# Kernel optimization log

Hardware: AMD Instinct MI355X
Metric: run time of the kernel (lower is better)

Reference implementation:

```python
import jax, jax.numpy as jnp
import numpy as np

B, T, H = 32, 2048, 1024
NEG = -1e9


def setup_inputs() -> dict:
    key = jax.random.key(0)
    ks = jax.random.split(key, 10)
    s = 1.0 / np.sqrt(H)
    return {
        "query": jax.random.normal(ks[0], (B, T, H), dtype=jnp.float32),
        "key_": jax.random.normal(ks[1], (B, T, H), dtype=jnp.float32),
        "value": jax.random.normal(ks[2], (B, T, H), dtype=jnp.float32),
        "lengths": jax.random.randint(ks[3], (B,), 1, T + 1),
        "Wq": jax.random.uniform(ks[4], (H, H), jnp.float32, -s, s),
        "bq": jax.random.uniform(ks[5], (H,), jnp.float32, -s, s),
        "Wk": jax.random.uniform(ks[6], (H, H), jnp.float32, -s, s),
        "bk": jax.random.uniform(ks[7], (H,), jnp.float32, -s, s),
        "Wz": jax.random.uniform(ks[8], (1, H), jnp.float32, -s, s),
        "bz": jax.random.uniform(ks[9], (1,), jnp.float32, -s, s),
    }


def reference(query, key_, value, lengths, Wq, bq, Wk, bk, Wz, bz):
    # projections: [B,T,H] @ [H,H]^T
    q = jnp.einsum("bth,oh->bto", query, Wq) + bq
    k = jnp.einsum("bth,oh->bto", key_, Wk) + bk
    # additive score -> [B,T,1]
    score = jnp.einsum("bth,oh->bto", jnp.tanh(q + k), Wz) + bz
    # mask positions t >= lengths[b]
    t_idx = jnp.arange(T)[None, :, None]  # [1,T,1]
    mask = t_idx >= lengths[:, None, None]  # [B,T,1]
    score = jnp.where(mask, NEG, score)
    att_weights = jax.nn.softmax(score, axis=1)  # [B,T,1]
    # weights^T [B,1,T] @ value [B,T,H] -> [B,1,H]
    att_value = jnp.einsum("bti,bth->bih", att_weights, value)
    return att_value, att_weights
```

## Files before the change

### kernel.cpp

```cpp
#include <hip/hip_runtime.h>
#include <hip/hip_bf16.h>

constexpr int TSEQ  = 2048;
constexpr int HDIM  = 1024;
constexpr int BATCH = 32;
constexpr int NPART = 16;
constexpr long ROWS = (long)BATCH * TSEQ;

constexpr int GBM = 256, GBN = 256, GBK = 64;
constexpr int GNT = (2 * HDIM) / GBK;

constexpr int BM = 128, BN = 128, BK = 64;
constexpr int NT = (2 * HDIM) / BK;

typedef __attribute__((ext_vector_type(8))) short bf16x8;
typedef __attribute__((ext_vector_type(8))) unsigned short u16x8;
typedef __attribute__((ext_vector_type(4))) float f32x4;

__device__ __forceinline__ unsigned short f2bf(float f) {
    union { float f; unsigned int u; } v; v.f = f;
    unsigned int r = v.u + 0x7FFFu + ((v.u >> 16) & 1u);
    return (unsigned short)(r >> 16);
}

__device__ __forceinline__ void gload16(const unsigned short* g, unsigned short* l) {
    __builtin_amdgcn_global_load_lds(
        (__attribute__((address_space(1))) void*)(g),
        (__attribute__((address_space(3))) void*)(l), 16, 0, 0);
}

__device__ __forceinline__ float fast_tanh(float x) {
    float e = __expf(2.0f * x);
    return 1.0f - 2.0f * __builtin_amdgcn_rcpf(e + 1.0f);
}

__global__ void convert_kernel(const float* __restrict__ q, const float* __restrict__ k,
                               const float* __restrict__ wq, const float* __restrict__ wk,
                               const int* __restrict__ lengths,
                               unsigned short* __restrict__ qb, unsigned short* __restrict__ kb,
                               unsigned short* __restrict__ wqb, unsigned short* __restrict__ wkb) {
    const long GQ = (ROWS * HDIM) / 8;
    const long GW = ((long)HDIM * HDIM) / 8;
    const long TOTAL = 2 * GQ + 2 * GW;
    const long stride = (long)gridDim.x * blockDim.x;
    for (long i = (long)blockIdx.x * blockDim.x + threadIdx.x; i < TOTAL; i += stride) {
        const float* src; unsigned short* dst; long off;
        if (i < 2 * GQ) {
            off = (i < GQ) ? i : i - GQ;
            const int row = (int)(off >> 7);
            if ((row & (TSEQ - 1)) >= lengths[row >> 11]) continue;
            src = (i < GQ) ? q : k;  dst = (i < GQ) ? qb : kb;
        } else if (i < 2 * GQ + GW) { src = wq; dst = wqb; off = i - 2 * GQ; }
        else                        { src = wk; dst = wkb; off = i - 2 * GQ - GW; }
        float4 v0 = *(const float4*)(src + off * 8);
        float4 v1 = *(const float4*)(src + off * 8 + 4);
        u16x8 o;
        o[0] = f2bf(v0.x); o[1] = f2bf(v0.y); o[2] = f2bf(v0.z); o[3] = f2bf(v0.w);
        o[4] = f2bf(v1.x); o[5] = f2bf(v1.y); o[6] = f2bf(v1.z); o[7] = f2bf(v1.w);
        *(u16x8*)(dst + off * 8) = o;
    }
}

__global__ __launch_bounds__(512, 2)
void score_gemm_256(const unsigned short* __restrict__ qb, const unsigned short* __restrict__ kb,
                    const unsigned short* __restrict__ wqb, const unsigned short* __restrict__ wkb,
                    const float* __restrict__ bq, const float* __restrict__ bk,
                    const float* __restrict__ Wz, const int* __restrict__ lengths,
                    float* __restrict__ scorePartial) {
    __shared__ unsigned short As[2 * 2 * 256 * 32];
    __shared__ unsigned short Bs[2 * 2 * 256 * 32];

    const int tid  = threadIdx.x;
    const int lane = tid & 63;
    const int wid  = tid >> 6;
    const int wr   = wid >> 2;
    const int wc   = wid & 3;

    const int x   = (int)blockIdx.x & 7;
    const int j   = (int)blockIdx.x >> 3;
    const int bat = j >> 2;
    const int nb  = j & 3;
    const int mb  = bat * 8 + ((x + bat) & 7);
    const long rowBase = (long)mb * GBM;
    const int  colBase = nb * GBN;

    if (((mb & 7) * GBM) >= lengths[bat]) return;

    const int frow = lane & 15;
    const int cs16 = (((lane >> 4) ^ ((frow >> 1) & 3)) << 4);
    const int sc8  = ((tid & 3) ^ ((tid >> 3) & 3)) * 8;

    f32x4 acc[8][4];
#pragma unroll
    for (int i = 0; i < 8; ++i)
#pragma unroll
        for (int j2 = 0; j2 < 4; ++j2) acc[i][j2] = (f32x4){0.f, 0.f, 0.f, 0.f};

    auto stage_half = [&](int n) {
        if (n >= 4 * GNT) return;
        const int tn   = n >> 2;
        const int part = n & 3;
        const int kh   = part >> 1;
        const int isB  = part & 1;
        const int kglob = tn * GBK + kh * 32;
        const unsigned short* src = (tn < 16) ? (isB ? wqb : qb) : (isB ? wkb : kb);
        const int ksrc = (tn < 16) ? kglob : (kglob - HDIM);
        const long rbase = isB ? (long)colBase : rowBase;
        unsigned short* lds = (isB ? Bs : As) + (tn & 1) * 16384 + kh * 8192;
#pragma unroll
        for (int jj = 0; jj < 2; ++jj) {
            const int row = jj * 128 + (tid >> 2);
            gload16(src + (rbase + row) * (long)HDIM + ksrc + sc8,
                    lds + jj * 4096 + (tid << 3));
        }
    };

    bf16x8 afr[4], bfr[4];
    auto ldA = [&](int d, int kh, int mh) {
        const char* p = (const char*)As + d * 32768 + kh * 16384;
#pragma unroll
        for (int mi = 0; mi < 4; ++mi) {
            const int row = wr * 128 + (mh * 4 + mi) * 16 + frow;
            afr[mi] = *(const bf16x8*)(p + row * 64 + cs16);
        }
    };
    auto ldB = [&](int d, int kh) {
        const char* p = (const char*)Bs + d * 32768 + kh * 16384;
#pragma unroll
        for (int ni = 0; ni < 4; ++ni) {
            const int row = wc * 64 + ni * 16 + frow;
            bfr[ni] = *(const bf16x8*)(p + row * 64 + cs16);
        }
    };

#pragma unroll
    for (int n = 0; n < 6; ++n) stage_half(n);
    asm volatile("s_waitcnt vmcnt(4)" ::: "memory");
    __builtin_amdgcn_s_barrier();

    for (int t = 0; t < GNT; ++t) {
        const int d = t & 1;
#pragma unroll
        for (int q = 0; q < 4; ++q) {
            const int kh = q >> 1, mh = q & 1;
            if (mh == 0) ldB(d, kh);
            ldA(d, kh, mh);
            stage_half(4 * t + q + 6);
            __builtin_amdgcn_s_barrier();
            asm volatile("s_waitcnt lgkmcnt(0)" ::: "memory");
            __builtin_amdgcn_sched_barrier(0);
            __builtin_amdgcn_s_setprio(1);
#pragma unroll
            for (int mi = 0; mi < 4; ++mi)
#pragma unroll
                for (int ni = 0; ni < 4; ++ni)
                    acc[mh * 4 + mi][ni] = __builtin_amdgcn_mfma_f32_16x16x32_bf16(
                        afr[mi], bfr[ni], acc[mh * 4 + mi][ni], 0, 0, 0);
            __builtin_amdgcn_s_setprio(0);
            if (q == 3) {
                if (t < GNT - 2)       asm volatile("s_waitcnt vmcnt(4)" ::: "memory");
                else if (t == GNT - 2) asm volatile("s_waitcnt vmcnt(0)" ::: "memory");
            }
            __builtin_amdgcn_s_barrier();
        }
    }

    float bias[4], wz[4];
#pragma unroll
    for (int ni = 0; ni < 4; ++ni) {
        const int o = colBase + wc * 64 + ni * 16 + frow;
        bias[ni] = bq[o] + bk[o];
        wz[ni]   = Wz[o];
    }
#pragma unroll
    for (int mi = 0; mi < 8; ++mi) {
#pragma unroll
        for (int jj = 0; jj < 4; ++jj) {
            float p = 0.f;
#pragma unroll
            for (int ni = 0; ni < 4; ++ni)
                p += fast_tanh(acc[mi][ni][jj] + bias[ni]) * wz[ni];
#pragma unroll
            for (int off = 1; off < 16; off <<= 1) p += __shfl_xor(p, off);
            if (frow == 0) {
                long r = rowBase + wr * 128 + mi * 16 + (lane >> 4) * 4 + jj;
                scorePartial[r * NPART + nb * 4 + wc] = p;
            }
        }
    }
}

__global__ __launch_bounds__(256, 2)
void score_gemm_fused(const float* __restrict__ query, const float* __restrict__ key_,
                      const float* __restrict__ Wq, const float* __restrict__ Wk,
                      const float* __restrict__ bq, const float* __restrict__ bk,
                      const float* __restrict__ Wz, const int* __restrict__ lengths,
                      float* __restrict__ scorePartial) {
    __shared__ unsigned short As[2][BM * BK];
    __shared__ unsigned short Bs[2][BN * BK];
    const int tid  = threadIdx.x;
    const int lane = tid & 63;
    const int wid  = tid >> 6;
    const int wr   = wid >> 1, wc = wid & 1;
    const int bid = blockIdx.x;
    const int nb  = bid & 7;
    const int mb  = bid >> 3;
    const long rowBase = (long)mb * BM;
    const int  colBase = nb * BN;
    if ((int)(rowBase & (TSEQ - 1)) >= lengths[(int)(rowBase >> 11)]) return;
    const int srow = tid >> 4;
    const int sc   = tid & 15;
    const int rA  = wr * 64 + (lane & 15);
    const int rB  = wc * 64 + (lane & 15);
    const int swz = (lane & 7) << 4;
    const int kb  = (lane >> 4) << 4;

    f32x4 acc[4][4];
#pragma unroll
    for (int i = 0; i < 4; i++)
#pragma unroll
        for (int j = 0; j < 4; j++) acc[i][j] = (f32x4){0.f, 0.f, 0.f, 0.f};

    float4 regA[8], regB[8];
    auto stage_load = [&](int kt) {
        const int kg = kt * BK;
        const float* baseA; const float* baseB; int koff;
        if (kg < HDIM) { baseA = query; baseB = Wq; koff = kg; }
        else           { baseA = key_;  baseB = Wk; koff = kg - HDIM; }
#pragma unroll
        for (int i = 0; i < 8; i++) {
            int row = i * 16 + srow;
            regA[i] = *(const float4*)(baseA + (rowBase + row) * (long)HDIM + koff + sc * 4);
            regB[i] = *(const float4*)(baseB + (long)(colBase + row) * HDIM + koff + sc * 4);
        }
    };
    auto stage_write = [&](int buf) {
#pragma unroll
        for (int i = 0; i < 8; i++) {
            int row = i * 16 + srow;
            int off = row * 128 + (((sc * 8)) ^ ((row & 7) << 4));
            ushort4 ha, hb;
            ha.x = f2bf(regA[i].x); ha.y = f2bf(regA[i].y);
            ha.z = f2bf(regA[i].z); ha.w = f2bf(regA[i].w);
            hb.x = f2bf(regB[i].x); hb.y = f2bf(regB[i].y);
            hb.z = f2bf(regB[i].z); hb.w = f2bf(regB[i].w);
            *(ushort4*)((char*)&As[buf][0] + off) = ha;
            *(ushort4*)((char*)&Bs[buf][0] + off) = hb;
        }
    };
    auto compute = [&](int buf) {
        const char* pA = (const char*)&As[buf][0];
        const char* pB = (const char*)&Bs[buf][0];
        bf16x8 a[4][2], b[4][2];
#pragma unroll
        for (int h = 0; h < 2; h++) {
#pragma unroll
            for (int mi = 0; mi < 4; mi++)
                a[mi][h] = *(const bf16x8*)(pA + (((rA + mi * 16) * 128 + h * 64 + kb) ^ swz));
#pragma unroll
            for (int ni = 0; ni < 4; ni++)
                b[ni][h] = *(const bf16x8*)(pB + (((rB + ni * 16) * 128 + h * 64 + kb) ^ swz));
        }
#pragma unroll
        for (int h = 0; h < 2; h++)
#pragma unroll
            for (int mi = 0; mi < 4; mi++)
#pragma unroll
                for (int ni = 0; ni < 4; ni++)
                    acc[mi][ni] = __builtin_amdgcn_mfma_f32_16x16x32_bf16(
                        a[mi][h], b[ni][h], acc[mi][ni], 0, 0, 0);
    };

    stage_load(0);
    stage_write(0);
    __syncthreads();
    int buf = 0;
    for (int kt = 1; kt < NT; ++kt) {
        stage_load(kt);
        compute(buf);
        stage_write(buf ^ 1);
        __syncthreads();
        buf ^= 1;
    }
    compute(buf);

    float bias[4], wz[4];
#pragma unroll
    for (int ni = 0; ni < 4; ni++) {
        int o = colBase + wc * 64 + ni * 16 + (lane & 15);
        bias[ni] = bq[o] + bk[o];
        wz[ni]   = Wz[o];
    }
#pragma unroll
    for (int mi = 0; mi < 4; mi++) {
#pragma unroll
        for (int j = 0; j < 4; j++) {
            float p = 0.f;
#pragma unroll
            for (int ni = 0; ni < 4; ni++) {
                float s = acc[mi][ni][j] + bias[ni];
                p += fast_tanh(s) * wz[ni];
            }
#pragma unroll
            for (int off = 1; off < 16; off <<= 1) p += __shfl_xor(p, off);
            if ((lane & 15) == 0) {
                long r = rowBase + wr * 64 + mi * 16 + (lane >> 4) * 4 + j;
                scorePartial[r * NPART + nb * 2 + wc] = p;
            }
        }
    }
}

__global__ void softmax_kernel(const float* __restrict__ sp, const float* __restrict__ bzp,
                               const int* __restrict__ lengths,
                               float* __restrict__ w_out, float* __restrict__ w_ws) {
    const int b = blockIdx.x;
    const int tid = threadIdx.x;
    const int len = lengths[b];
    const float bz = bzp[0];
    float sv[8];
    float m = -3.0e38f;
#pragma unroll
    for (int i = 0; i < 8; i++) {
        int t = i * 256 + tid;
        const float4* p = (const float4*)(sp + ((long)b * TSEQ + t) * NPART);
        float s;
        if (t >= len) {
            s = -1e9f;
        } else {
            float4 a = p[0], c = p[1], d = p[2], e = p[3];
            s = (a.x + a.y + a.z + a.w) + (c.x + c.y + c.z + c.w) +
                (d.x + d.y + d.z + d.w) + (e.x + e.y + e.z + e.w) + bz;
        }
        sv[i] = s;
        m = fmaxf(m, s);
    }
    __shared__ float redm[4];
    __shared__ float reds[4];
    for (int off = 32; off; off >>= 1) m = fmaxf(m, __shfl_xor(m, off));
    if ((tid & 63) == 0) redm[tid >> 6] = m;
    __syncthreads();
    m = fmaxf(fmaxf(redm[0], redm[1]), fmaxf(redm[2], redm[3]));
    float sum = 0.f;
    float ev[8];
#pragma unroll
    for (int i = 0; i < 8; i++) {
        ev[i] = expf(sv[i] - m);
        sum += ev[i];
    }
    for (int off = 32; off; off >>= 1) sum += __shfl_xor(sum, off);
    if ((tid & 63) == 0) reds[tid >> 6] = sum;
    __syncthreads();
    sum = reds[0] + reds[1] + reds[2] + reds[3];
    const float inv = 1.0f / sum;
#pragma unroll
    for (int i = 0; i < 8; i++) {
        int t = i * 256 + tid;
        float w = ev[i] * inv;
        w_out[(long)b * TSEQ + t] = w;
        w_ws[(long)b * TSEQ + t] = w;
    }
}

__global__ void pv_partial(const float* __restrict__ w, const float* __restrict__ value,
                           const int* __restrict__ lengths, float* __restrict__ part) {
    const int ntc = gridDim.x;
    const int tchunk = TSEQ / ntc;
    const int tc = blockIdx.x;
    const int hc = blockIdx.y;
    const int b  = blockIdx.z;
    const int tid = threadIdx.x;
    const int h = hc * 512 + tid * 4;
    float* dst = part + ((long)(b * ntc + tc)) * HDIM + h;
    if (tc * tchunk >= lengths[b]) {
        *(float4*)dst = (float4){0.f, 0.f, 0.f, 0.f};
        return;
    }
    __shared__ float sw[128];
    if (tid < tchunk) sw[tid] = w[(long)b * TSEQ + tc * tchunk + tid];
    __syncthreads();
    float4 acc = {0.f, 0.f, 0.f, 0.f};
    const float* vbase = value + ((long)b * TSEQ + tc * tchunk) * HDIM + h;
#pragma unroll 4
    for (int tt = 0; tt < tchunk; ++tt) {
        float4 v = *(const float4*)(vbase + (long)tt * HDIM);
        float wv = sw[tt];
        acc.x += wv * v.x; acc.y += wv * v.y;
        acc.z += wv * v.z; acc.w += wv * v.w;
    }
    *(float4*)dst = acc;
}

__global__ void pv_reduce(const float* __restrict__ part, float* __restrict__ out, int ntc) {
    const int b = blockIdx.x;
    const int tid = threadIdx.x;
    const int h = tid * 4;
    float4 acc = {0.f, 0.f, 0.f, 0.f};
    for (int tc = 0; tc < ntc; ++tc) {
        float4 v = *(const float4*)(part + ((long)(b * ntc + tc)) * HDIM + h);
        acc.x += v.x; acc.y += v.y; acc.z += v.z; acc.w += v.w;
    }
    *(float4*)(out + (long)b * HDIM + h) = acc;
}

extern "C" void kernel_launch(void* const* d_in, const int* in_sizes, int n_in,
                              void* d_out, int out_size, void* d_ws, size_t ws_size,
                              hipStream_t stream) {
    const float* query   = (const float*)d_in[0];
    const float* key_    = (const float*)d_in[1];
    const float* value   = (const float*)d_in[2];
    const int*   lengths = (const int*)d_in[3];
    const float* Wq = (const float*)d_in[4];
    const float* bq = (const float*)d_in[5];
    const float* Wk = (const float*)d_in[6];
    const float* bk = (const float*)d_in[7];
    const float* Wz = (const float*)d_in[8];
    const float* bz = (const float*)d_in[9];
    float* out = (float*)d_out;

    const long QB_B  = ROWS * HDIM * 2;
    const long WB_B  = (long)HDIM * HDIM * 2;
    const long SP_B  = ROWS * NPART * 4;
    const long WW_B  = ROWS * 4;
    const long P2_B  = (long)BATCH * 32 * HDIM * 4;
    const long NEED  = 2 * QB_B + 2 * WB_B + SP_B + WW_B + P2_B;

    if ((long)ws_size >= NEED) {
        char* w = (char*)d_ws;
        unsigned short* qb  = (unsigned short*)w;            w += QB_B;
        unsigned short* kb  = (unsigned short*)w;            w += QB_B;
        unsigned short* wqb = (unsigned short*)w;            w += WB_B;
        unsigned short* wkb = (unsigned short*)w;            w += WB_B;
        float* sp   = (float*)w;                             w += SP_B;
        float* wbuf = (float*)w;                             w += WW_B;
        float* p2   = (float*)w;

        convert_kernel<<<dim3(4096), dim3(256), 0, stream>>>(
            query, key_, Wq, Wk, lengths, qb, kb, wqb, wkb);
        score_gemm_256<<<dim3(1024), dim3(512), 0, stream>>>(
            qb, kb, wqb, wkb, bq, bk, Wz, lengths, sp);
        softmax_kernel<<<dim3(BATCH), dim3(256), 0, stream>>>(
            sp, bz, lengths, out + BATCH * HDIM, wbuf);
        pv_partial<<<dim3(32, 2, BATCH), dim3(128), 0, stream>>>(wbuf, value, lengths, p2);
        pv_reduce<<<dim3(BATCH), dim3(256), 0, stream>>>(p2, out, 32);
    } else {
        float* sp   = (float*)d_ws;
        float* wbuf = sp + ROWS * NPART;
        float* p2   = wbuf + ROWS;
        score_gemm_fused<<<dim3(4096), dim3(256), 0, stream>>>(
            query, key_, Wq, Wk, bq, bk, Wz, lengths, sp);
        softmax_kernel<<<dim3(BATCH), dim3(256), 0, stream>>>(
            sp, bz, lengths, out + BATCH * HDIM, wbuf);
        pv_partial<<<dim3(16, 2, BATCH), dim3(128), 0, stream>>>(wbuf, value, lengths, p2);
        pv_reduce<<<dim3(BATCH), dim3(256), 0, stream>>>(p2, out, 16);
    }
}
```

Before: 334.8 us.

## Restructure score GEMM main loop into register double-buffered 4-stage LDS pipeline

Replaces the 2-buffer, 4-quarter-per-tile GEMM loop with a 4-slot LDS ring of K=32 half-tiles. Each stage loads A and B together, and A/B fragments are double-buffered in registers so the next phase's LDS reads overlap the current MFMA block. This leaves one barrier per phase instead of two and issues 32 MFMAs per phase. The aim is less barrier and LDS-latency stall, at the cost of more VGPRs for the doubled fragments, which may hurt occupancy under launch_bounds(512,2).

```diff
diff --git a/kernel.cpp b/kernel.cpp
--- a/kernel.cpp
+++ b/kernel.cpp
@@ -67,8 +67,8 @@
                     const float* __restrict__ bq, const float* __restrict__ bk,
                     const float* __restrict__ Wz, const int* __restrict__ lengths,
                     float* __restrict__ scorePartial) {
-    __shared__ unsigned short As[2 * 2 * 256 * 32];
-    __shared__ unsigned short Bs[2 * 2 * 256 * 32];
+    __shared__ unsigned short As[4 * 256 * 32];
+    __shared__ unsigned short Bs[4 * 256 * 32];
 
     const int tid  = threadIdx.x;
     const int lane = tid & 63;
@@ -89,6 +89,8 @@
     const int frow = lane & 15;
     const int cs16 = (((lane >> 4) ^ ((frow >> 1) & 3)) << 4);
     const int sc8  = ((tid & 3) ^ ((tid >> 3) & 3)) * 8;
+    const int rowA = wr * 128 + frow;
+    const int rowB = wc * 64 + frow;
 
     f32x4 acc[8][4];
 #pragma unroll
@@ -96,74 +98,68 @@
 #pragma unroll
         for (int j2 = 0; j2 < 4; ++j2) acc[i][j2] = (f32x4){0.f, 0.f, 0.f, 0.f};
 
-    auto stage_half = [&](int n) {
-        if (n >= 4 * GNT) return;
-        const int tn   = n >> 2;
-        const int part = n & 3;
-        const int kh   = part >> 1;
-        const int isB  = part & 1;
-        const int kglob = tn * GBK + kh * 32;
-        const unsigned short* src = (tn < 16) ? (isB ? wqb : qb) : (isB ? wkb : kb);
-        const int ksrc = (tn < 16) ? kglob : (kglob - HDIM);
-        const long rbase = isB ? (long)colBase : rowBase;
-        unsigned short* lds = (isB ? Bs : As) + (tn & 1) * 16384 + kh * 8192;
+    auto stage = [&](int n) {
+        const int tn = n >> 1;
+        const unsigned short* asrc = (tn < 16) ? qb : kb;
+        const unsigned short* bsrc = (tn < 16) ? wqb : wkb;
+        const int ksrc = (tn & 15) * 64 + (n & 1) * 32 + sc8;
+        unsigned short* ldsA = As + (n & 3) * 8192;
+        unsigned short* ldsB = Bs + (n & 3) * 8192;
 #pragma unroll
         for (int jj = 0; jj < 2; ++jj) {
             const int row = jj * 128 + (tid >> 2);
-            gload16(src + (rbase + row) * (long)HDIM + ksrc + sc8,
-                    lds + jj * 4096 + (tid << 3));
+            gload16(asrc + (rowBase + row) * (long)HDIM + ksrc, ldsA + jj * 4096 + (tid << 3));
+            gload16(bsrc + (long)(colBase + row) * HDIM + ksrc, ldsB + jj * 4096 + (tid << 3));
         }
     };
 
-    bf16x8 afr[4], bfr[4];
-    auto ldA = [&](int d, int kh, int mh) {
-        const char* p = (const char*)As + d * 32768 + kh * 16384;
-#pragma unroll
-        for (int mi = 0; mi < 4; ++mi) {
-            const int row = wr * 128 + (mh * 4 + mi) * 16 + frow;
-            afr[mi] = *(const bf16x8*)(p + row * 64 + cs16);
-        }
-    };
-    auto ldB = [&](int d, int kh) {
-        const char* p = (const char*)Bs + d * 32768 + kh * 16384;
-#pragma unroll
-        for (int ni = 0; ni < 4; ++ni) {
-            const int row = wc * 64 + ni * 16 + frow;
-            bfr[ni] = *(const bf16x8*)(p + row * 64 + cs16);
-        }
-    };
-
-#pragma unroll
-    for (int n = 0; n < 6; ++n) stage_half(n);
+    bf16x8 fA0[8], fB0[4], fA1[8], fB1[4];
+
+    stage(0); stage(1); stage(2);
     asm volatile("s_waitcnt vmcnt(4)" ::: "memory");
     __builtin_amdgcn_s_barrier();
-
-    for (int t = 0; t < GNT; ++t) {
-        const int d = t & 1;
-#pragma unroll
-        for (int q = 0; q < 4; ++q) {
-            const int kh = q >> 1, mh = q & 1;
-            if (mh == 0) ldB(d, kh);
-            ldA(d, kh, mh);
-            stage_half(4 * t + q + 6);
-            __builtin_amdgcn_s_barrier();
-            asm volatile("s_waitcnt lgkmcnt(0)" ::: "memory");
-            __builtin_amdgcn_sched_barrier(0);
-            __builtin_amdgcn_s_setprio(1);
-#pragma unroll
-            for (int mi = 0; mi < 4; ++mi)
-#pragma unroll
-                for (int ni = 0; ni < 4; ++ni)
-                    acc[mh * 4 + mi][ni] = __builtin_amdgcn_mfma_f32_16x16x32_bf16(
-                        afr[mi], bfr[ni], acc[mh * 4 + mi][ni], 0, 0, 0);
-            __builtin_amdgcn_s_setprio(0);
-            if (q == 3) {
-                if (t < GNT - 2)       asm volatile("s_waitcnt vmcnt(4)" ::: "memory");
-                else if (t == GNT - 2) asm volatile("s_waitcnt vmcnt(0)" ::: "memory");
-            }
-            __builtin_amdgcn_s_barrier();
-        }
-    }
+#pragma unroll
+    for (int mi = 0; mi < 8; ++mi)
+        fA0[mi] = *(const bf16x8*)((const char*)As + (rowA + mi * 16) * 64 + cs16);
+#pragma unroll
+    for (int ni = 0; ni < 4; ++ni)
+        fB0[ni] = *(const bf16x8*)((const char*)Bs + (rowB + ni * 16) * 64 + cs16);
+
+#define PHASE(H, BUFN, FAC, FBC, FAN, FBN)                                       \
+    {                                                                            \
+        const int h_ = (H);                                                      \
+        if (h_ <= 60) stage(h_ + 3);                                             \
+        if (h_ <= 62) {                                                          \
+            const char* pA_ = (const char*)As + (BUFN) * 16384;                  \
+            const char* pB_ = (const char*)Bs + (BUFN) * 16384;                  \
+            _Pragma("unroll") for (int mi = 0; mi < 8; ++mi)                     \
+                FAN[mi] = *(const bf16x8*)(pA_ + (rowA + mi * 16) * 64 + cs16);  \
+            _Pragma("unroll") for (int ni = 0; ni < 4; ++ni)                     \
+                FBN[ni] = *(const bf16x8*)(pB_ + (rowB + ni * 16) * 64 + cs16);  \
+            asm volatile("s_waitcnt lgkmcnt(12)" ::: "memory");                  \
+        } else {                                                                 \
+            asm volatile("s_waitcnt lgkmcnt(0)" ::: "memory");                   \
+        }                                                                        \
+        __builtin_amdgcn_sched_barrier(0);                                       \
+        __builtin_amdgcn_s_setprio(1);                                           \
+        _Pragma("unroll") for (int mi = 0; mi < 8; ++mi)                         \
+            _Pragma("unroll") for (int ni = 0; ni < 4; ++ni)                     \
+                acc[mi][ni] = __builtin_amdgcn_mfma_f32_16x16x32_bf16(           \
+                    FAC[mi], FBC[ni], acc[mi][ni], 0, 0, 0);                     \
+        __builtin_amdgcn_s_setprio(0);                                           \
+        if (h_ <= 60)      asm volatile("s_waitcnt vmcnt(4)" ::: "memory");      \
+        else if (h_ == 61) asm volatile("s_waitcnt vmcnt(0)" ::: "memory");      \
+        __builtin_amdgcn_s_barrier();                                            \
+    }
+
+    for (int i = 0; i < 16; ++i) {
+        const int h = i * 4;
+        PHASE(h + 0, 1, fA0, fB0, fA1, fB1);
+        PHASE(h + 1, 2, fA1, fB1, fA0, fB0);
+        PHASE(h + 2, 3, fA0, fB0, fA1, fB1);
+        PHASE(h + 3, 0, fA1, fB1, fA0, fB0);
+    }
+#undef PHASE
 
     float bias[4], wz[4];
 #pragma unroll
```

Measured after the change: 449.2 us. 1.34x slower.
